# Optimization experiments

Hardware: AMD Instinct MI355X
Metric: run time of the kernel (lower is better)

## Reference

```python
import jax, jax.numpy as jnp
import numpy as np

ALPHA = 0.2  # LeakyReLU negative slope
EPS = 1e-16


def setup_inputs() -> dict:
    key = jax.random.key(0)
    k0, k1, k2, k3 = jax.random.split(key, 4)
    N, E, F_in, F_out, HEADS = 50000, 1600000, 256, 128, 4
    H = jax.random.normal(k0, (N, F_in), dtype=jnp.float32)
    edge_index = jax.random.randint(k1, (2, E), 0, N)  # row0=src, row1=dst
    # Xavier-ish scaled params
    W = jax.random.normal(k2, (HEADS, F_out, F_in), dtype=jnp.float32) * (1.0 / np.sqrt(F_in))
    a = jax.random.normal(k3, (HEADS, 2 * F_out), dtype=jnp.float32) * 0.1
    bias = jnp.zeros((F_out,), dtype=jnp.float32)
    return {"H": H, "edge_index": edge_index, "W": W, "a": a, "bias": bias}


def reference(H, edge_index, W, a, bias):
    """GAT layer: per-head edge attention + segment softmax over src + SpMM, mean over heads.

    H: [N, F_in]; edge_index: [2, E]; W: [heads, F_out, F_in]; a: [heads, 2*F_out]; bias: [F_out]
    Note: a(concat(h_src, h_dst)) == h_src @ a[:F_out] + h_dst @ a[F_out:], so we compute the
    two per-node scores once on nodes instead of materializing the E x 2*F_out concat.
    """
    N = H.shape[0]
    heads, F_out, _ = W.shape
    src, dst = edge_index[0], edge_index[1]
    outs = []
    for h in range(heads):
        Ht = H @ W[h].T                      # [N, F_out]
        s_src = Ht @ a[h, :F_out]            # [N]
        s_dst = Ht @ a[h, F_out:]            # [N]
        e = s_src[src] + s_dst[dst]          # [E]
        e = jnp.where(e > 0, e, ALPHA * e)   # LeakyReLU
        # segment softmax over src nodes (matches scatter amax + scatter_add)
        e_max = jax.ops.segment_max(e, src, num_segments=N)    # [N], -inf for isolated nodes
        e_exp = jnp.exp(e - e_max[src])                         # [E]
        denom = jax.ops.segment_sum(e_exp, src, num_segments=N) # [N]
        attn = e_exp / (denom[src] + EPS)                       # [E]
        # sparse.mm(attention, Ht): out[i] = sum_{(i,j) in E} attn_ij * Ht[j]
        out = jax.ops.segment_sum(attn[:, None] * Ht[dst], src, num_segments=N)  # [N, F_out]
        outs.append(out)
    final = jnp.mean(jnp.stack(outs, axis=0), axis=0) + bias
    return final
```

## Files before the change

kernel.cpp:

```cpp
#include <hip/hip_runtime.h>

#define ALPHA 0.2f
#define EPS 1e-16f

static constexpr int F_IN = 256;
static constexpr int F_OUT = 128;
static constexpr int HEADS = 4;
static constexpr int COLS = HEADS * F_OUT;

typedef __bf16 bf16x8 __attribute__((ext_vector_type(8)));
typedef float f32x4 __attribute__((ext_vector_type(4)));

static __device__ __forceinline__ unsigned short f2bf(float f) {
  unsigned int u = __float_as_uint(f);
  unsigned int r = (u + 0x7FFFu + ((u >> 16) & 1u)) >> 16;
  return (unsigned short)r;
}
static __device__ __forceinline__ float bf_lo(unsigned int u) {
  return __uint_as_float(u << 16);
}
static __device__ __forceinline__ float bf_hi(unsigned int u) {
  return __uint_as_float(u & 0xFFFF0000u);
}

__global__ __launch_bounds__(256) void k_wprep(const float* __restrict__ W,
                                               const float* __restrict__ a,
                                               unsigned short* __restrict__ Wb,
                                               float* __restrict__ u) {
  if (blockIdx.x < 128) {
    const int i = blockIdx.x * 256 + threadIdx.x;
    const float4 v = ((const float4*)W)[i];
    ((ushort4*)Wb)[i] = make_ushort4(f2bf(v.x), f2bf(v.y), f2bf(v.z), f2bf(v.w));
  } else {
    const int b = blockIdx.x - 128;
    const int h = b >> 1, dual = b & 1;
    const int k = threadIdx.x;
    float s = 0.f;
    for (int f = 0; f < F_OUT; ++f)
      s = fmaf(a[h * 2 * F_OUT + dual * F_OUT + f], W[((size_t)h * F_OUT + f) * F_IN + k], s);
    u[b * F_IN + k] = s;
  }
}

__global__ __launch_bounds__(256) void k_pre(const float4* __restrict__ H4,
    const float* __restrict__ u, unsigned short* __restrict__ Hb,
    float4* __restrict__ ssrc4, unsigned char* __restrict__ rec, int N, int CB,
    const int* __restrict__ src, int* __restrict__ cnt,
    unsigned short* __restrict__ rank, int E) {
  if ((int)blockIdx.x >= CB) {
    int i = (blockIdx.x - CB) * 256 + threadIdx.x;
    const int stride = 1024 * 256;
    for (; i < E; i += stride) rank[i] = (unsigned short)atomicAdd(&cnt[src[i]], 1);
    return;
  }
  const int wv = threadIdx.x >> 6, lane = threadIdx.x & 63;
  const int n = ((int)blockIdx.x << 2) + wv;
  if (n >= N) return;
  const float4 hv = H4[(size_t)n * 64 + lane];
  *((ushort4*)(Hb + (size_t)n * F_IN) + lane) =
      make_ushort4(f2bf(hv.x), f2bf(hv.y), f2bf(hv.z), f2bf(hv.w));
  float p[8];
#pragma unroll
  for (int c = 0; c < 8; ++c) {
    const float4 uv = *(const float4*)&u[c * F_IN + (lane << 2)];
    p[c] = fmaf(hv.x, uv.x, fmaf(hv.y, uv.y, fmaf(hv.z, uv.z, hv.w * uv.w)));
  }
#pragma unroll
  for (int c = 0; c < 8; ++c)
#pragma unroll
    for (int m = 1; m < 64; m <<= 1) p[c] += __shfl_xor(p[c], m);
  if (lane == 0) {
    ssrc4[n] = make_float4(p[0], p[2], p[4], p[6]);
    *(float4*)&rec[(size_t)n * 32] = make_float4(p[1], p[3], p[5], p[7]);
  }
}

__global__ __launch_bounds__(256) void k_gemm_q(const unsigned short* __restrict__ A,
                                                const unsigned short* __restrict__ B,
                                                unsigned char* __restrict__ Hq,
                                                unsigned char* __restrict__ rec, int N) {
  __shared__ __bf16 As[128][40];
  __shared__ __bf16 Bs[128][40];
  const int t = threadIdx.x;
  const int w = t >> 6, l = t & 63;
  const int wr = w >> 1, wc = w & 1;
  const int m0 = blockIdx.y << 7, n0 = blockIdx.x << 7;
  const int lr = t >> 1, seg16 = (t & 1) << 4;
  f32x4 acc[4][4] = {};
  for (int k0 = 0; k0 < F_IN; k0 += 32) {
    int ar = m0 + lr; if (ar >= N) ar = N - 1;
    const uint4 a0 = *(const uint4*)&A[(size_t)ar * F_IN + k0 + seg16];
    const uint4 a1 = *(const uint4*)&A[(size_t)ar * F_IN + k0 + seg16 + 8];
    const uint4 b0 = *(const uint4*)&B[(size_t)(n0 + lr) * F_IN + k0 + seg16];
    const uint4 b1 = *(const uint4*)&B[(size_t)(n0 + lr) * F_IN + k0 + seg16 + 8];
    __syncthreads();
    *(uint4*)&As[lr][seg16] = a0;  *(uint4*)&As[lr][seg16 + 8] = a1;
    *(uint4*)&Bs[lr][seg16] = b0;  *(uint4*)&Bs[lr][seg16 + 8] = b1;
    __syncthreads();
    const int kb = (l >> 4) << 3;
    bf16x8 af[4], bf_[4];
#pragma unroll
    for (int mi = 0; mi < 4; ++mi)
      af[mi] = *(const bf16x8*)&As[(wr << 6) + (mi << 4) + (l & 15)][kb];
#pragma unroll
    for (int ni = 0; ni < 4; ++ni)
      bf_[ni] = *(const bf16x8*)&Bs[(wc << 6) + (ni << 4) + (l & 15)][kb];
#pragma unroll
    for (int mi = 0; mi < 4; ++mi)
#pragma unroll
      for (int ni = 0; ni < 4; ++ni)
        acc[mi][ni] = __builtin_amdgcn_mfma_f32_16x16x32_bf16(af[mi], bf_[ni], acc[mi][ni], 0, 0, 0);
  }
  const int bxg = (blockIdx.x << 1) + wc;
#pragma unroll
  for (int mi = 0; mi < 4; ++mi)
#pragma unroll
    for (int r = 0; r < 4; ++r) {
      float mx = 0.f;
#pragma unroll
      for (int ni = 0; ni < 4; ++ni) mx = fmaxf(mx, fabsf(acc[mi][ni][r]));
#pragma unroll
      for (int m = 1; m < 16; m <<= 1) mx = fmaxf(mx, __shfl_xor(mx, m));
      const int row = m0 + (wr << 6) + (mi << 4) + ((l >> 4) << 2) + r;
      if (row < N) {
        const float inv = (mx > 0.f) ? 127.f / mx : 0.f;
        if ((l & 15) == 0)
          *(unsigned short*)&rec[(size_t)row * 32 + 16 + (bxg << 1)] = f2bf(mx * (1.f / 127.f));
        unsigned int pk = 0;
#pragma unroll
        for (int ni = 0; ni < 4; ++ni) {
          float tq = fminf(fmaxf(rintf(acc[mi][ni][r] * inv), -127.f), 127.f);
          pk |= ((unsigned int)((int)tq & 255)) << (8 * ni);
        }
        *(unsigned int*)&Hq[(size_t)row * 512 + (bxg << 6) + ((l & 15) << 2)] = pk;
      }
    }
}

__global__ __launch_bounds__(1024) void k_scan1(int* __restrict__ cnt,
                                                int* __restrict__ bsum, int N) {
  __shared__ int ws[16];
  const int t = threadIdx.x, g = blockIdx.x * 1024 + t;
  const int lane = t & 63, w = t >> 6;
  int v = (g < N) ? cnt[g] : 0;
#pragma unroll
  for (int o = 1; o < 64; o <<= 1) {
    const int y = __shfl_up(v, o);
    if (lane >= o) v += y;
  }
  if (lane == 63) ws[w] = v;
  __syncthreads();
  if (w == 0) {
    int s = (lane < 16) ? ws[lane] : 0;
#pragma unroll
    for (int o = 1; o < 16; o <<= 1) {
      const int y = __shfl_up(s, o);
      if (lane >= o) s += y;
    }
    if (lane < 16) ws[lane] = s;
  }
  __syncthreads();
  v += (w > 0) ? ws[w - 1] : 0;
  if (g < N) cnt[g] = v;
  if (t == 1023) bsum[blockIdx.x] = v;
}

__global__ __launch_bounds__(1024) void k_scan3(const int* __restrict__ part,
                                                const int* __restrict__ bsum,
                                                int* __restrict__ off, int N, int nb) {
  __shared__ int sbuf[256];
  const int t = threadIdx.x;
  if (t < 64) {
    int carry = 0;
    for (int base = 0; base < nb; base += 64) {
      int v = (base + t < nb) ? bsum[base + t] : 0;
#pragma unroll
      for (int o = 1; o < 64; o <<= 1) {
        const int y = __shfl_up(v, o);
        if (t >= o) v += y;
      }
      v += carry;
      if (base + t < nb) sbuf[base + t] = v;
      carry = __shfl(v, 63);
    }
  }
  __syncthreads();
  const int g = blockIdx.x * 1024 + t;
  if (g == 0) off[0] = 0;
  if (g < N) off[g + 1] = part[g] + (blockIdx.x ? sbuf[blockIdx.x - 1] : 0);
}

__global__ void k_scatter(const int* __restrict__ src, const int* __restrict__ dst,
                          const int* __restrict__ off, const unsigned short* __restrict__ rank,
                          unsigned short* __restrict__ csr_dst, int E) {
  int i = blockIdx.x * blockDim.x + threadIdx.x;
  const int stride = gridDim.x * blockDim.x;
  for (; i < E; i += stride)
    csr_dst[off[src[i]] + rank[i]] = (unsigned short)dst[i];
}

__global__ __launch_bounds__(256) void k_spmm(const uint2* __restrict__ Hq2,
    const float4* __restrict__ ssrc4, const unsigned char* __restrict__ rec,
    const int* __restrict__ off, const unsigned short* __restrict__ csr_dst,
    const float* __restrict__ bias, float* __restrict__ out, int N) {
  __shared__ float wbuf[4][8][72];
  __shared__ int   ibuf[4][64];
  const int wv = threadIdx.x >> 6;
  const int lane = threadIdx.x & 63;
  const int n = (blockIdx.x << 2) + wv;
  if (n >= N) return;
  const int hg = lane >> 4;
  const int b8 = lane >> 3;
  const float4 ss4 = ssrc4[n];
  float den4[4] = {};
  float acc[8] = {};
  const int beg = off[n], end = off[n + 1];
  for (int c0 = beg; c0 < end; c0 += 64) {
    const int cnt = min(64, end - c0);
    if (lane < cnt) {
      const int d = csr_dst[c0 + lane];
      ibuf[wv][lane] = d << 6;
      const float4 sd4 = *(const float4*)&rec[(size_t)d * 32];
      const uint4  sc  = *(const uint4*)&rec[(size_t)d * 32 + 16];
      float e0 = ss4.x + sd4.x; e0 = fmaxf(e0, ALPHA * e0);
      float e1 = ss4.y + sd4.y; e1 = fmaxf(e1, ALPHA * e1);
      float e2 = ss4.z + sd4.z; e2 = fmaxf(e2, ALPHA * e2);
      float e3 = ss4.w + sd4.w; e3 = fmaxf(e3, ALPHA * e3);
      const float w0 = __expf(e0), w1 = __expf(e1), w2 = __expf(e2), w3 = __expf(e3);
      den4[0] += w0; den4[1] += w1; den4[2] += w2; den4[3] += w3;
      wbuf[wv][0][lane] = w0 * bf_lo(sc.x); wbuf[wv][1][lane] = w0 * bf_hi(sc.x);
      wbuf[wv][2][lane] = w1 * bf_lo(sc.y); wbuf[wv][3][lane] = w1 * bf_hi(sc.y);
      wbuf[wv][4][lane] = w2 * bf_lo(sc.z); wbuf[wv][5][lane] = w2 * bf_hi(sc.z);
      wbuf[wv][6][lane] = w3 * bf_lo(sc.w); wbuf[wv][7][lane] = w3 * bf_hi(sc.w);
    }
#pragma unroll 8
    for (int j = 0; j < cnt; ++j) {
      const float wgt = wbuf[wv][b8][j];
      const int db = ibuf[wv][j];
      const uint2 q = Hq2[db + lane];
      acc[0] = fmaf(wgt, (float)(char)(q.x),       acc[0]);
      acc[1] = fmaf(wgt, (float)(char)(q.x >> 8),  acc[1]);
      acc[2] = fmaf(wgt, (float)(char)(q.x >> 16), acc[2]);
      acc[3] = fmaf(wgt, (float)(char)(q.x >> 24), acc[3]);
      acc[4] = fmaf(wgt, (float)(char)(q.y),       acc[4]);
      acc[5] = fmaf(wgt, (float)(char)(q.y >> 8),  acc[5]);
      acc[6] = fmaf(wgt, (float)(char)(q.y >> 16), acc[6]);
      acc[7] = fmaf(wgt, (float)(char)(q.y >> 24), acc[7]);
    }
  }
#pragma unroll
  for (int k = 0; k < 4; ++k)
#pragma unroll
    for (int m = 1; m < 64; m <<= 1) den4[k] += __shfl_xor(den4[k], m);
  const float r = 1.f / (den4[hg] + EPS);
#pragma unroll
  for (int i = 0; i < 8; ++i) acc[i] *= r;
#pragma unroll
  for (int i = 0; i < 8; ++i) {
    acc[i] += __shfl_xor(acc[i], 16);
    acc[i] += __shfl_xor(acc[i], 32);
  }
  if (lane < 16) {
    const int base = ((lane >> 3) & 1) * 64 + ((lane & 7) << 1);
#pragma unroll
    for (int k = 0; k < 4; ++k) {
      const float2 b2 = *(const float2*)&bias[base + k * 16];
      *(float2*)&out[(size_t)n * F_OUT + base + k * 16] =
          make_float2(0.25f * acc[k] + b2.x, 0.25f * acc[k + 4] + b2.y);
    }
  }
}

extern "C" void kernel_launch(void* const* d_in, const int* in_sizes, int n_in,
                              void* d_out, int out_size, void* d_ws, size_t ws_size,
                              hipStream_t stream) {
  const float* H    = (const float*)d_in[0];
  const int*   ei   = (const int*)d_in[1];
  const float* W    = (const float*)d_in[2];
  const float* a    = (const float*)d_in[3];
  const float* bias = (const float*)d_in[4];
  const int N = in_sizes[0] / F_IN;
  const int E = in_sizes[1] / 2;
  const int* src = ei;
  const int* dst = ei + E;

  char* ws = (char*)d_ws;
  size_t o = 0;
  auto alloc = [&](size_t bytes) -> void* {
    void* p = ws + o;
    o = (o + bytes + 255) & ~(size_t)255;
    return p;
  };
  unsigned short* Hb  = (unsigned short*)alloc((size_t)N * F_IN * 2);
  unsigned short* Wb  = (unsigned short*)alloc((size_t)COLS * F_IN * 2);
  unsigned char*  Hq  = (unsigned char*)alloc((size_t)N * COLS);
  float* uvec = (float*)alloc(8 * F_IN * sizeof(float));
  float* ssrc = (float*)alloc((size_t)N * HEADS * sizeof(float));
  unsigned char* rec = (unsigned char*)alloc((size_t)N * 32);
  int*   cnt  = (int*)alloc((size_t)N * sizeof(int));
  int*   off  = (int*)alloc(((size_t)N + 1) * sizeof(int));
  unsigned short* csr = (unsigned short*)alloc((size_t)E * sizeof(unsigned short));
  unsigned short* rank = (unsigned short*)alloc((size_t)E * sizeof(unsigned short));
  const int nb = (N + 1023) / 1024;
  int*   bsum = (int*)alloc((size_t)nb * sizeof(int));

  hipMemsetAsync(cnt, 0, (size_t)N * sizeof(int), stream);

  k_wprep<<<136, 256, 0, stream>>>(W, a, Wb, uvec);
  const int CB = (N + 3) / 4;
  k_pre<<<CB + 1024, 256, 0, stream>>>((const float4*)H, uvec, Hb,
                                       (float4*)ssrc, rec, N, CB,
                                       src, cnt, rank, E);
  dim3 ggrid(COLS / 128, (N + 127) / 128);
  k_gemm_q<<<ggrid, 256, 0, stream>>>(Hb, Wb, Hq, rec, N);
  k_scan1<<<nb, 1024, 0, stream>>>(cnt, bsum, N);
  k_scan3<<<nb, 1024, 0, stream>>>(cnt, bsum, off, N, nb);
  k_scatter<<<1024, 256, 0, stream>>>(src, dst, off, rank, csr, E);
  k_spmm<<<(N + 3) / 4, 256, 0, stream>>>((const uint2*)Hq, (const float4*)ssrc,
                                          rec, off, csr, bias, (float*)d_out, N);
}
```

Measured before the change: 300.8 us.

## Remap GEMM blocks per XCD and store int8 as offset-binary to cheapen SpMM decode

The GEMM launch becomes a 1D grid whose block IDs are remapped so that consecutive tiles of the same row block land on the same XCD, improving L2 reuse of the A rows across the four column tiles. Quantized values are now stored offset by +128 (unsigned bytes), so the SpMM inner loop can use unsigned byte extraction instead of sign-extending casts. The offset is removed at the end by subtracting 128 times the accumulated weight sum. This adds one accumulator per lane, and the subtraction of the bias term can cost some floating-point accuracy.

```diff
diff --git a/kernel.cpp b/kernel.cpp
--- a/kernel.cpp
+++ b/kernel.cpp
@@ -81,10 +81,17 @@
                                                 unsigned char* __restrict__ rec, int N) {
   __shared__ __bf16 As[128][40];
   __shared__ __bf16 Bs[128][40];
+  const int T = gridDim.x;
+  const int q8 = T >> 3, r8 = T & 7;
+  const int xcd = blockIdx.x & 7, ii = blockIdx.x >> 3;
+  const int gp = (xcd < r8) ? xcd * (q8 + 1) + ii
+                            : r8 * (q8 + 1) + (xcd - r8) * q8 + ii;
+  const int by = gp >> 2;
+  const int bx = gp & 3;
   const int t = threadIdx.x;
   const int w = t >> 6, l = t & 63;
   const int wr = w >> 1, wc = w & 1;
-  const int m0 = blockIdx.y << 7, n0 = blockIdx.x << 7;
+  const int m0 = by << 7, n0 = bx << 7;
   const int lr = t >> 1, seg16 = (t & 1) << 4;
   f32x4 acc[4][4] = {};
   for (int k0 = 0; k0 < F_IN; k0 += 32) {
@@ -111,7 +118,7 @@
       for (int ni = 0; ni < 4; ++ni)
         acc[mi][ni] = __builtin_amdgcn_mfma_f32_16x16x32_bf16(af[mi], bf_[ni], acc[mi][ni], 0, 0, 0);
   }
-  const int bxg = (blockIdx.x << 1) + wc;
+  const int bxg = (bx << 1) + wc;
 #pragma unroll
   for (int mi = 0; mi < 4; ++mi)
 #pragma unroll
@@ -130,7 +137,7 @@
 #pragma unroll
         for (int ni = 0; ni < 4; ++ni) {
           float tq = fminf(fmaxf(rintf(acc[mi][ni][r] * inv), -127.f), 127.f);
-          pk |= ((unsigned int)((int)tq & 255)) << (8 * ni);
+          pk |= ((unsigned int)(((int)tq + 128) & 255)) << (8 * ni);
         }
         *(unsigned int*)&Hq[(size_t)row * 512 + (bxg << 6) + ((l & 15) << 2)] = pk;
       }
@@ -214,6 +221,7 @@
   const float4 ss4 = ssrc4[n];
   float den4[4] = {};
   float acc[8] = {};
+  float sw = 0.f;
   const int beg = off[n], end = off[n + 1];
   for (int c0 = beg; c0 < end; c0 += 64) {
     const int cnt = min(64, end - c0);
@@ -238,14 +246,15 @@
       const float wgt = wbuf[wv][b8][j];
       const int db = ibuf[wv][j];
       const uint2 q = Hq2[db + lane];
-      acc[0] = fmaf(wgt, (float)(char)(q.x),       acc[0]);
-      acc[1] = fmaf(wgt, (float)(char)(q.x >> 8),  acc[1]);
-      acc[2] = fmaf(wgt, (float)(char)(q.x >> 16), acc[2]);
-      acc[3] = fmaf(wgt, (float)(char)(q.x >> 24), acc[3]);
-      acc[4] = fmaf(wgt, (float)(char)(q.y),       acc[4]);
-      acc[5] = fmaf(wgt, (float)(char)(q.y >> 8),  acc[5]);
-      acc[6] = fmaf(wgt, (float)(char)(q.y >> 16), acc[6]);
-      acc[7] = fmaf(wgt, (float)(char)(q.y >> 24), acc[7]);
+      sw += wgt;
+      acc[0] = fmaf(wgt, (float)(q.x & 0xffu),         acc[0]);
+      acc[1] = fmaf(wgt, (float)((q.x >> 8) & 0xffu),  acc[1]);
+      acc[2] = fmaf(wgt, (float)((q.x >> 16) & 0xffu), acc[2]);
+      acc[3] = fmaf(wgt, (float)(q.x >> 24),           acc[3]);
+      acc[4] = fmaf(wgt, (float)(q.y & 0xffu),         acc[4]);
+      acc[5] = fmaf(wgt, (float)((q.y >> 8) & 0xffu),  acc[5]);
+      acc[6] = fmaf(wgt, (float)((q.y >> 16) & 0xffu), acc[6]);
+      acc[7] = fmaf(wgt, (float)(q.y >> 24),           acc[7]);
     }
   }
 #pragma unroll
@@ -253,8 +262,9 @@
 #pragma unroll
     for (int m = 1; m < 64; m <<= 1) den4[k] += __shfl_xor(den4[k], m);
   const float r = 1.f / (den4[hg] + EPS);
-#pragma unroll
-  for (int i = 0; i < 8; ++i) acc[i] *= r;
+  const float corr = 128.f * sw;
+#pragma unroll
+  for (int i = 0; i < 8; ++i) acc[i] = (acc[i] - corr) * r;
 #pragma unroll
   for (int i = 0; i < 8; ++i) {
     acc[i] += __shfl_xor(acc[i], 16);
@@ -311,8 +321,8 @@
   k_pre<<<CB + 1024, 256, 0, stream>>>((const float4*)H, uvec, Hb,
                                        (float4*)ssrc, rec, N, CB,
                                        src, cnt, rank, E);
-  dim3 ggrid(COLS / 128, (N + 127) / 128);
-  k_gemm_q<<<ggrid, 256, 0, stream>>>(Hb, Wb, Hq, rec, N);
+  const int nb128 = (N + 127) / 128;
+  k_gemm_q<<<4 * nb128, 256, 0, stream>>>(Hb, Wb, Hq, rec, N);
   k_scan1<<<nb, 1024, 0, stream>>>(cnt, bsum, N);
   k_scan3<<<nb, 1024, 0, stream>>>(cnt, bsum, off, N, nb);
   k_scatter<<<1024, 256, 0, stream>>>(src, dst, off, rank, csr, E);
```

Measured after the change: 300.8 us. Within noise of the previous version (-0.0%).
